# Performance work log

Measured on AMD Instinct MI355X. Metric: run time of the kernel, lower is better.

Reference implementation:

```python
import jax, jax.numpy as jnp
import numpy as np

N = 50000        # nodes
E = 400000       # edges
CHUNK = 100      # per-modality input dim
NCH = 2          # number of chunks (modalities)
OUT = 96         # out_chunks
HID = NCH * OUT  # m_hidden = 192
NCLS = 2         # edge classes
EPS = 1e-5


def layer_norm(x, g, b):
    m = jnp.mean(x, axis=-1, keepdims=True)
    v = jnp.var(x, axis=-1, keepdims=True)
    return (x - m) * jax.lax.rsqrt(v + EPS) * g + b


def setup_inputs() -> dict:
    key = jax.random.key(0)
    ks = jax.random.split(key, 20)
    inp = {}
    inp["h"] = jax.random.normal(ks[0], (N, NCH * CHUNK), dtype=jnp.float32)
    inp["dist"] = jax.random.uniform(ks[1], (E,), dtype=jnp.float32)
    inp["src"] = jax.random.randint(ks[2], (E,), 0, N)
    inp["dst"] = jax.random.randint(ks[3], (E,), 0, N)
    # projector params (equal chunk sizes -> stacked): Linear(100,96)+LayerNorm(96)
    s = 1.0 / np.sqrt(CHUNK)
    inp["proj_W"] = jax.random.uniform(ks[4], (NCH, CHUNK, OUT), minval=-s, maxval=s, dtype=jnp.float32)
    inp["proj_b"] = jax.random.uniform(ks[5], (NCH, OUT), minval=-s, maxval=s, dtype=jnp.float32)
    inp["proj_g"] = jnp.ones((NCH, OUT), jnp.float32)
    inp["proj_beta"] = jnp.zeros((NCH, OUT), jnp.float32)
    # 2 GcnSAGE layers actually run (m_layers-1): Linear(2*192, 192) + LayerNorm(192)
    sg = 1.0 / np.sqrt(2 * HID)
    inp["gcn_W"] = jax.random.uniform(ks[6], (2, 2 * HID, HID), minval=-sg, maxval=sg, dtype=jnp.float32)
    inp["gcn_b"] = jax.random.uniform(ks[7], (2, HID), minval=-sg, maxval=sg, dtype=jnp.float32)
    inp["gcn_g"] = jnp.ones((2, HID), jnp.float32)
    inp["gcn_beta"] = jnp.zeros((2, HID), jnp.float32)
    # edge MLP predictor: 192 -> 96 -> 2
    s1 = 1.0 / np.sqrt(HID)
    s2 = 1.0 / np.sqrt(HID // 2)
    inp["ep_W1"] = jax.random.uniform(ks[8], (HID, HID // 2), minval=-s1, maxval=s1, dtype=jnp.float32)
    inp["ep_b1"] = jax.random.uniform(ks[9], (HID // 2,), minval=-s1, maxval=s1, dtype=jnp.float32)
    inp["ep_W2"] = jax.random.uniform(ks[10], (HID // 2, NCLS), minval=-s2, maxval=s2, dtype=jnp.float32)
    inp["ep_b2"] = jax.random.uniform(ks[11], (NCLS,), minval=-s2, maxval=s2, dtype=jnp.float32)
    return inp


def reference(h, dist, proj_W, proj_b, proj_g, proj_beta,
              gcn_W, gcn_b, gcn_g, gcn_beta,
              ep_W1, ep_b1, ep_W2, ep_b2, src, dst):
    # InputProjector: per-chunk Linear + LayerNorm + LeakyReLU, concat
    x = h.reshape(N, NCH, CHUNK)
    y = jnp.einsum('ncd,cde->nce', x, proj_W) + proj_b
    y = jax.nn.leaky_relu(layer_norm(y, proj_g, proj_beta), negative_slope=0.01)
    hh = y.reshape(N, HID)

    # 1/in_degree norm (inf -> 0)
    deg = jax.ops.segment_sum(jnp.ones((E,), hh.dtype), dst, num_segments=N)
    norm = jnp.where(deg > 0, 1.0 / deg, 0.0)[:, None]

    # m_layers - 1 = 2 GcnSAGE layers: ah = sum_{u->v} h_u * dist_e
    for l in range(2):
        msg = hh[src] * dist[:, None]                       # [E, HID]
        ah = jax.ops.segment_sum(msg, dst, num_segments=N)  # [N, HID]
        hc = jnp.concatenate([hh, ah * norm], axis=1)       # [N, 2*HID]
        hh = hc @ gcn_W[l] + gcn_b[l]
        hh = jax.nn.relu(layer_norm(hh, gcn_g[l], gcn_beta[l]))

    # edge scoring: W2(relu(W1(h_src * h_dst)))
    he = hh[src] * hh[dst]                                   # [E, HID]
    score = jax.nn.relu(he @ ep_W1 + ep_b1) @ ep_W2 + ep_b2  # [E, 2]
    return score
```

## Files before the change

### kernel.cpp

```cpp
#include <hip/hip_runtime.h>
#include <math.h>

#define N_NODES 50000
#define N_EDGES 400000
#define CHUNK   100
#define NCH     2
#define OUTC    96
#define HID     192
#define HID2    384
#define EPS     1e-5f

typedef __bf16 bf16x8 __attribute__((ext_vector_type(8)));
typedef float  f32x4  __attribute__((ext_vector_type(4)));

__device__ inline unsigned short f2bf(float f) {
    unsigned int u = __float_as_uint(f);
    unsigned int r = (u + 0x7FFFu + ((u >> 16) & 1u)) >> 16;
    return (unsigned short)r;
}

#define W1T_SZ (96 * 192)
__global__ void prep_w1t(const float* __restrict__ W1, unsigned short* __restrict__ w1t)
{
    int i = blockIdx.x * 256 + threadIdx.x;
    if (i < W1T_SZ) {
        int j = i / HID, k = i % HID;
        w1t[i] = f2bf(W1[k * OUTC + j]);
    }
}

__global__ __launch_bounds__(192) void proj_kernel(
    const float* __restrict__ h, const float* __restrict__ W,
    const float* __restrict__ b, const float* __restrict__ g,
    const float* __restrict__ beta, float* __restrict__ hh)
{
    __shared__ float xs[16][NCH * CHUNK];
    __shared__ float red[2][16][2][6];
    __shared__ float mv[2][16][2];
    const int tid = threadIdx.x;
    const int nbase = blockIdx.x * 16;

    for (int i = tid; i < 16 * 50; i += 192) {
        int row = i / 50, seg = i % 50;
        int n = nbase + row;
        float4 v = make_float4(0.f, 0.f, 0.f, 0.f);
        if (n < N_NODES) v = *(const float4*)&h[(size_t)n * (NCH * CHUNK) + seg * 4];
        *(float4*)&xs[row][seg * 4] = v;
    }
    __syncthreads();

    const int c = tid / OUTC, j = tid % OUTC;
    const float* wc = &W[c * CHUNK * OUTC];

    float acc[16];
    float bb = b[c * OUTC + j];
    #pragma unroll
    for (int i = 0; i < 16; ++i) acc[i] = bb;

    for (int d = 0; d < CHUNK; d += 4) {
        float w0 = wc[(d + 0) * OUTC + j];
        float w1 = wc[(d + 1) * OUTC + j];
        float w2 = wc[(d + 2) * OUTC + j];
        float w3 = wc[(d + 3) * OUTC + j];
        #pragma unroll
        for (int i = 0; i < 16; ++i) {
            float4 hv = *(const float4*)&xs[i][c * CHUNK + d];
            acc[i] += hv.x * w0 + hv.y * w1 + hv.z * w2 + hv.w * w3;
        }
    }
    __syncthreads();
    float* ys = &xs[0][0];
    #pragma unroll
    for (int i = 0; i < 16; ++i) ys[i * HID + c * OUTC + j] = acc[i];
    __syncthreads();
    {
        int grp = tid / 6, q = tid % 6;
        int gi = grp >> 1, gc = grp & 1;
        float s = 0.f, s2 = 0.f;
        #pragma unroll
        for (int t = 0; t < 16; ++t) {
            float v = ys[gi * HID + gc * OUTC + q + 6 * t];
            s += v; s2 += v * v;
        }
        red[0][gi][gc][q] = s; red[1][gi][gc][q] = s2;
    }
    __syncthreads();
    if (tid < 32) {
        int gi = tid >> 1, gc = tid & 1;
        float s = 0.f, s2 = 0.f;
        #pragma unroll
        for (int q = 0; q < 6; ++q) { s += red[0][gi][gc][q]; s2 += red[1][gi][gc][q]; }
        float mean = s * (1.f / 96.f);
        float var  = s2 * (1.f / 96.f) - mean * mean;
        mv[0][gi][gc] = mean;
        mv[1][gi][gc] = rsqrtf(var + EPS);
    }
    __syncthreads();
    float gg = g[c * OUTC + j], be = beta[c * OUTC + j];
    #pragma unroll
    for (int i = 0; i < 16; ++i) {
        int n = nbase + i;
        if (n < N_NODES) {
            float y = (acc[i] - mv[0][i][c]) * mv[1][i][c] * gg + be;
            y = (y < 0.f) ? 0.01f * y : y;
            hh[(size_t)n * HID + c * OUTC + j] = y;
        }
    }
}

__global__ void zero_deg_kernel(int* __restrict__ deg)
{
    int i = blockIdx.x * blockDim.x + threadIdx.x;
    if (i < N_NODES) deg[i] = 0;
}

__global__ void count_kernel(const int* __restrict__ dst, int* __restrict__ deg)
{
    int e = blockIdx.x * blockDim.x + threadIdx.x;
    if (e < N_EDGES) atomicAdd(&deg[dst[e]], 1);
}

__global__ __launch_bounds__(1024) void scan_kernel(
    const int* __restrict__ deg, int* __restrict__ rowstart,
    int* __restrict__ cursor, float* __restrict__ norm)
{
    __shared__ int sums[1024];
    const int t = threadIdx.x;
    const int L = (N_NODES + 1023) / 1024;
    int lo = t * L, hi = min(lo + L, N_NODES);
    int s = 0;
    for (int i = lo; i < hi; ++i) s += deg[i];
    sums[t] = s;
    __syncthreads();
    if (t == 0) {
        int run = 0;
        for (int i = 0; i < 1024; ++i) { int v = sums[i]; sums[i] = run; run += v; }
        rowstart[N_NODES] = run;
    }
    __syncthreads();
    int off = sums[t];
    for (int i = lo; i < hi; ++i) {
        int d = deg[i];
        rowstart[i] = off;
        cursor[i]   = off;
        norm[i]     = (d > 0) ? 1.f / (float)d : 0.f;
        off += d;
    }
}

__global__ void fill_kernel(const int* __restrict__ src, const int* __restrict__ dst,
                            const float* __restrict__ dist, int* __restrict__ cursor,
                            int* __restrict__ eidx, int* __restrict__ csr_src,
                            float* __restrict__ csr_dist)
{
    int e = blockIdx.x * blockDim.x + threadIdx.x;
    if (e < N_EDGES) {
        int pos = atomicAdd(&cursor[dst[e]], 1);
        eidx[pos]     = e;
        csr_src[pos]  = src[e];
        csr_dist[pos] = dist[e];
    }
}

__global__ __launch_bounds__(256) void aggregate_kernel(
    const float* __restrict__ hh, const int* __restrict__ csr_src,
    const float* __restrict__ csr_dist, const int* __restrict__ rowstart,
    const float* __restrict__ norm, float* __restrict__ ahn)
{
    const int wave = threadIdx.x >> 6;
    const int lane = threadIdx.x & 63;
    const int v = blockIdx.x * 4 + wave;
    if (v >= N_NODES) return;
    const int r0 = rowstart[v], r1 = rowstart[v + 1];
    const bool act = (lane < 48);
    const int g4 = (act ? lane : 0) * 4;

    f32x4 a = (f32x4){0.f, 0.f, 0.f, 0.f};
    int k = r0;
    for (; k + 1 < r1; k += 2) {
        int   s0 = csr_src[k],   s1 = csr_src[k + 1];
        float d0 = csr_dist[k],  d1 = csr_dist[k + 1];
        f32x4 h0 = *(const f32x4*)&hh[(size_t)s0 * HID + g4];
        f32x4 h1 = *(const f32x4*)&hh[(size_t)s1 * HID + g4];
        a += h0 * d0;
        a += h1 * d1;
    }
    if (k < r1) {
        int s0 = csr_src[k];
        float d0 = csr_dist[k];
        f32x4 h0 = *(const f32x4*)&hh[(size_t)s0 * HID + g4];
        a += h0 * d0;
    }
    if (act) {
        float nm = norm[v];
        a *= nm;
        *(f32x4*)&ahn[(size_t)v * HID + g4] = a;
    }
}

__global__ __launch_bounds__(256, 1) void update_kernel(
    float* __restrict__ hh, const float* __restrict__ ahn,
    const float* __restrict__ W, const float* __restrict__ b,
    const float* __restrict__ g, const float* __restrict__ beta)
{
    __shared__ float red[64][4][2];
    const int tid  = threadIdx.x;
    const int lane = tid & 63;
    const int wv   = tid >> 6;
    const int j0   = __builtin_amdgcn_readfirstlane(wv * 48);
    const int node = blockIdx.x * 64 + lane;
    const bool valid = (node < N_NODES);
    const int nclamp = valid ? node : (N_NODES - 1);

    const float* __restrict__ xrow = &hh[(size_t)nclamp * HID];
    const float* __restrict__ arow = &ahn[(size_t)nclamp * HID];

    f32x4 a0, a1, a2, a3, a4, a5, a6, a7, a8, a9, a10, a11;
    {
        const f32x4* bj = (const f32x4*)&b[j0];
        a0 = bj[0]; a1 = bj[1]; a2 = bj[2];  a3 = bj[3];  a4 = bj[4];   a5 = bj[5];
        a6 = bj[6]; a7 = bj[7]; a8 = bj[8];  a9 = bj[9];  a10 = bj[10]; a11 = bj[11];
    }

#define UPD_STEP(xs, krow)                                                   \
    {                                                                        \
        const f32x4* __restrict__ wr = (const f32x4*)&W[(size_t)(krow) * HID + j0]; \
        a0  += (xs) * wr[0];  a1  += (xs) * wr[1];  a2  += (xs) * wr[2];     \
        a3  += (xs) * wr[3];  a4  += (xs) * wr[4];  a5  += (xs) * wr[5];     \
        a6  += (xs) * wr[6];  a7  += (xs) * wr[7];  a8  += (xs) * wr[8];     \
        a9  += (xs) * wr[9];  a10 += (xs) * wr[10]; a11 += (xs) * wr[11];    \
    }

    for (int k = 0; k < HID; k += 4) {
        float4 xv = *(const float4*)&xrow[k];
        UPD_STEP(xv.x, k + 0)
        UPD_STEP(xv.y, k + 1)
        UPD_STEP(xv.z, k + 2)
        UPD_STEP(xv.w, k + 3)
    }
    for (int k = 0; k < HID; k += 4) {
        float4 xv = *(const float4*)&arow[k];
        UPD_STEP(xv.x, HID + k + 0)
        UPD_STEP(xv.y, HID + k + 1)
        UPD_STEP(xv.z, HID + k + 2)
        UPD_STEP(xv.w, HID + k + 3)
    }
#undef UPD_STEP

    float s = 0.f, s2 = 0.f;
#define UPD_SUM(av) { s += av[0] + av[1] + av[2] + av[3];                          \
                      s2 += av[0]*av[0] + av[1]*av[1] + av[2]*av[2] + av[3]*av[3]; }
    UPD_SUM(a0) UPD_SUM(a1) UPD_SUM(a2) UPD_SUM(a3) UPD_SUM(a4) UPD_SUM(a5)
    UPD_SUM(a6) UPD_SUM(a7) UPD_SUM(a8) UPD_SUM(a9) UPD_SUM(a10) UPD_SUM(a11)
#undef UPD_SUM
    red[lane][wv][0] = s;
    red[lane][wv][1] = s2;
    __syncthreads();
    float st = 0.f, s2t = 0.f;
    #pragma unroll
    for (int w2 = 0; w2 < 4; ++w2) { st += red[lane][w2][0]; s2t += red[lane][w2][1]; }
    float mean = st * (1.f / HID);
    float var  = s2t * (1.f / HID) - mean * mean;
    float rstd = rsqrtf(var + EPS);

    if (valid) {
        float* __restrict__ orow = &hh[(size_t)node * HID + j0];
        const f32x4* __restrict__ gj = (const f32x4*)&g[j0];
        const f32x4* __restrict__ ej = (const f32x4*)&beta[j0];
#define UPD_OUT(av, jv)                                                      \
    {                                                                        \
        f32x4 gv = gj[jv], bv = ej[jv], o;                                   \
        o[0] = fmaxf((av[0] - mean) * rstd * gv[0] + bv[0], 0.f);            \
        o[1] = fmaxf((av[1] - mean) * rstd * gv[1] + bv[1], 0.f);            \
        o[2] = fmaxf((av[2] - mean) * rstd * gv[2] + bv[2], 0.f);            \
        o[3] = fmaxf((av[3] - mean) * rstd * gv[3] + bv[3], 0.f);            \
        *(f32x4*)&orow[(jv) * 4] = o;                                        \
    }
        UPD_OUT(a0, 0)  UPD_OUT(a1, 1)  UPD_OUT(a2, 2)  UPD_OUT(a3, 3)
        UPD_OUT(a4, 4)  UPD_OUT(a5, 5)  UPD_OUT(a6, 6)  UPD_OUT(a7, 7)
        UPD_OUT(a8, 8)  UPD_OUT(a9, 9)  UPD_OUT(a10, 10) UPD_OUT(a11, 11)
#undef UPD_OUT
    }
}

__global__ __launch_bounds__(256) void edge_mfma_kernel(
    const float* __restrict__ hh, const int* __restrict__ src, const int* __restrict__ dst,
    const int* __restrict__ eidx,
    const unsigned short* __restrict__ w1t, const float* __restrict__ b1,
    const float* __restrict__ W2, const float* __restrict__ b2,
    float* __restrict__ out)
{
    __shared__ unsigned short he[64][200];
    __shared__ int sidx[64], didx[64], eor[64];
    const int tid = threadIdx.x;
    const int ebase = blockIdx.x * 64;

    if (tid < 64) {
        int e = eidx[ebase + tid];
        eor[tid] = e;
        sidx[tid] = src[e];
        didx[tid] = dst[e];
    }
    __syncthreads();

    for (int idx = tid; idx < 64 * 48; idx += 256) {
        int slot = idx / 48, q = idx % 48;
        f32x4 sv = *(const f32x4*)&hh[(size_t)sidx[slot] * HID + q * 4];
        f32x4 dv = *(const f32x4*)&hh[(size_t)didx[slot] * HID + q * 4];
        f32x4 pv = sv * dv;
        ushort4 o;
        o.x = f2bf(pv[0]); o.y = f2bf(pv[1]); o.z = f2bf(pv[2]); o.w = f2bf(pv[3]);
        *(ushort4*)&he[slot][q * 4] = o;
    }
    __syncthreads();

    const int w    = tid >> 6;
    const int lane = tid & 63;
    const int lo   = lane & 15;
    const int hi   = lane >> 4;

    f32x4 acc[6];
    #pragma unroll
    for (int nt = 0; nt < 6; ++nt) acc[nt] = (f32x4){0.f, 0.f, 0.f, 0.f};

    #pragma unroll
    for (int kt = 0; kt < 6; ++kt) {
        const int k0 = kt * 32 + hi * 8;
        bf16x8 af = *(const bf16x8*)&he[w * 16 + lo][k0];
        #pragma unroll
        for (int nt = 0; nt < 6; ++nt) {
            bf16x8 bfr = *(const bf16x8*)&w1t[(size_t)(nt * 16 + lo) * HID + k0];
            acc[nt] = __builtin_amdgcn_mfma_f32_16x16x32_bf16(af, bfr, acc[nt], 0, 0, 0);
        }
    }

    float b1c[6], w20[6], w21[6];
    #pragma unroll
    for (int nt = 0; nt < 6; ++nt) {
        int col = nt * 16 + lo;
        b1c[nt] = b1[col];
        w20[nt] = W2[col * 2 + 0];
        w21[nt] = W2[col * 2 + 1];
    }
    float bb0 = b2[0], bb1 = b2[1];
    #pragma unroll
    for (int reg = 0; reg < 4; ++reg) {
        float p0 = 0.f, p1 = 0.f;
        #pragma unroll
        for (int nt = 0; nt < 6; ++nt) {
            float hv = fmaxf(acc[nt][reg] + b1c[nt], 0.f);
            p0 += hv * w20[nt];
            p1 += hv * w21[nt];
        }
        #pragma unroll
        for (int off = 1; off < 16; off <<= 1) {
            p0 += __shfl_xor(p0, off, 64);
            p1 += __shfl_xor(p1, off, 64);
        }
        if (lo == 0) {
            int row = hi * 4 + reg;
            int e = eor[w * 16 + row];
            out[(size_t)e * 2 + 0] = p0 + bb0;
            out[(size_t)e * 2 + 1] = p1 + bb1;
        }
    }
}

extern "C" void kernel_launch(void* const* d_in, const int* in_sizes, int n_in,
                              void* d_out, int out_size, void* d_ws, size_t ws_size,
                              hipStream_t stream)
{
    const float* h         = (const float*)d_in[0];
    const float* dist      = (const float*)d_in[1];
    const int*   src       = (const int*)  d_in[2];
    const int*   dst       = (const int*)  d_in[3];
    const float* proj_W    = (const float*)d_in[4];
    const float* proj_b    = (const float*)d_in[5];
    const float* proj_g    = (const float*)d_in[6];
    const float* proj_beta = (const float*)d_in[7];
    const float* gcn_W     = (const float*)d_in[8];
    const float* gcn_b     = (const float*)d_in[9];
    const float* gcn_g     = (const float*)d_in[10];
    const float* gcn_beta  = (const float*)d_in[11];
    const float* ep_W1     = (const float*)d_in[12];
    const float* ep_b1     = (const float*)d_in[13];
    const float* ep_W2     = (const float*)d_in[14];
    const float* ep_b2     = (const float*)d_in[15];
    float* out = (float*)d_out;

    char* p = (char*)d_ws;
    float* hh  = (float*)p;  p += (size_t)N_NODES * HID * sizeof(float);
    float* ahn = (float*)p;  p += (size_t)N_NODES * HID * sizeof(float);
    float* nrm = (float*)p;  p += (size_t)N_NODES * sizeof(float);
    int* deg      = (int*)p; p += (size_t)N_NODES * sizeof(int);
    int* rowstart = (int*)p; p += (size_t)(N_NODES + 1) * sizeof(int);
    int* cursor   = (int*)p; p += (size_t)N_NODES * sizeof(int);
    int* eidx     = (int*)p; p += (size_t)N_EDGES * sizeof(int);
    int* csr_src  = (int*)p; p += (size_t)N_EDGES * sizeof(int);
    float* csr_dist = (float*)p; p += (size_t)N_EDGES * sizeof(float);
    p = (char*)(((uintptr_t)p + 255) & ~(uintptr_t)255);
    unsigned short* w1t = (unsigned short*)p; p += (size_t)W1T_SZ * sizeof(unsigned short);

    prep_w1t<<<(W1T_SZ + 255) / 256, 256, 0, stream>>>(ep_W1, w1t);
    proj_kernel<<<(N_NODES + 15) / 16, 192, 0, stream>>>(
        h, proj_W, proj_b, proj_g, proj_beta, hh);
    zero_deg_kernel<<<(N_NODES + 255) / 256, 256, 0, stream>>>(deg);
    count_kernel<<<(N_EDGES + 255) / 256, 256, 0, stream>>>(dst, deg);
    scan_kernel<<<1, 1024, 0, stream>>>(deg, rowstart, cursor, nrm);
    fill_kernel<<<(N_EDGES + 255) / 256, 256, 0, stream>>>(
        src, dst, dist, cursor, eidx, csr_src, csr_dist);
    for (int l = 0; l < 2; ++l) {
        aggregate_kernel<<<(N_NODES + 3) / 4, 256, 0, stream>>>(
            hh, csr_src, csr_dist, rowstart, nrm, ahn);
        update_kernel<<<(N_NODES + 63) / 64, 256, 0, stream>>>(
            hh, ahn, gcn_W + (size_t)l * HID2 * HID, gcn_b + l * HID,
            gcn_g + l * HID, gcn_beta + l * HID);
    }
    edge_mfma_kernel<<<N_EDGES / 64, 256, 0, stream>>>(
        hh, src, dst, eidx, w1t, ep_b1, ep_W2, ep_b2, out);
}
```

Measured before the change: 750.3 us.

## Split update GEMM K-dimension across two wave groups and unroll aggregation by four

```diff
diff --git a/kernel.cpp b/kernel.cpp
--- a/kernel.cpp
+++ b/kernel.cpp
@@ -177,15 +177,19 @@
 
     f32x4 a = (f32x4){0.f, 0.f, 0.f, 0.f};
     int k = r0;
-    for (; k + 1 < r1; k += 2) {
-        int   s0 = csr_src[k],   s1 = csr_src[k + 1];
-        float d0 = csr_dist[k],  d1 = csr_dist[k + 1];
+    for (; k + 3 < r1; k += 4) {
+        int   s0 = csr_src[k],   s1 = csr_src[k+1],  s2 = csr_src[k+2],  s3 = csr_src[k+3];
+        float d0 = csr_dist[k],  d1 = csr_dist[k+1], d2 = csr_dist[k+2], d3 = csr_dist[k+3];
         f32x4 h0 = *(const f32x4*)&hh[(size_t)s0 * HID + g4];
         f32x4 h1 = *(const f32x4*)&hh[(size_t)s1 * HID + g4];
+        f32x4 h2 = *(const f32x4*)&hh[(size_t)s2 * HID + g4];
+        f32x4 h3 = *(const f32x4*)&hh[(size_t)s3 * HID + g4];
         a += h0 * d0;
         a += h1 * d1;
-    }
-    if (k < r1) {
+        a += h2 * d2;
+        a += h3 * d3;
+    }
+    for (; k < r1; ++k) {
         int s0 = csr_src[k];
         float d0 = csr_dist[k];
         f32x4 h0 = *(const f32x4*)&hh[(size_t)s0 * HID + g4];
@@ -198,28 +202,34 @@
     }
 }
 
-__global__ __launch_bounds__(256, 1) void update_kernel(
+__global__ __launch_bounds__(512) void update_kernel(
     float* __restrict__ hh, const float* __restrict__ ahn,
     const float* __restrict__ W, const float* __restrict__ b,
     const float* __restrict__ g, const float* __restrict__ beta)
 {
+    __shared__ float mrg[4][48][64];
     __shared__ float red[64][4][2];
     const int tid  = threadIdx.x;
     const int lane = tid & 63;
     const int wv   = tid >> 6;
-    const int j0   = __builtin_amdgcn_readfirstlane(wv * 48);
+    const int wb   = wv & 3;
+    const int half = wv >> 2;
+    const int j0   = __builtin_amdgcn_readfirstlane(wb * 48);
     const int node = blockIdx.x * 64 + lane;
     const bool valid = (node < N_NODES);
     const int nclamp = valid ? node : (N_NODES - 1);
 
-    const float* __restrict__ xrow = &hh[(size_t)nclamp * HID];
-    const float* __restrict__ arow = &ahn[(size_t)nclamp * HID];
+    const float* __restrict__ xrow = half ? &ahn[(size_t)nclamp * HID]
+                                          : &hh[(size_t)nclamp * HID];
+    const int kbase = half * HID;
 
     f32x4 a0, a1, a2, a3, a4, a5, a6, a7, a8, a9, a10, a11;
-    {
+    if (half == 0) {
         const f32x4* bj = (const f32x4*)&b[j0];
         a0 = bj[0]; a1 = bj[1]; a2 = bj[2];  a3 = bj[3];  a4 = bj[4];   a5 = bj[5];
         a6 = bj[6]; a7 = bj[7]; a8 = bj[8];  a9 = bj[9];  a10 = bj[10]; a11 = bj[11];
+    } else {
+        a0=a1=a2=a3=a4=a5=a6=a7=a8=a9=a10=a11 = (f32x4){0.f,0.f,0.f,0.f};
     }
 
 #define UPD_STEP(xs, krow)                                                   \
@@ -230,43 +240,57 @@
         a6  += (xs) * wr[6];  a7  += (xs) * wr[7];  a8  += (xs) * wr[8];     \
         a9  += (xs) * wr[9];  a10 += (xs) * wr[10]; a11 += (xs) * wr[11];    \
     }
-
     for (int k = 0; k < HID; k += 4) {
         float4 xv = *(const float4*)&xrow[k];
-        UPD_STEP(xv.x, k + 0)
-        UPD_STEP(xv.y, k + 1)
-        UPD_STEP(xv.z, k + 2)
-        UPD_STEP(xv.w, k + 3)
-    }
-    for (int k = 0; k < HID; k += 4) {
-        float4 xv = *(const float4*)&arow[k];
-        UPD_STEP(xv.x, HID + k + 0)
-        UPD_STEP(xv.y, HID + k + 1)
-        UPD_STEP(xv.z, HID + k + 2)
-        UPD_STEP(xv.w, HID + k + 3)
+        UPD_STEP(xv.x, kbase + k + 0)
+        UPD_STEP(xv.y, kbase + k + 1)
+        UPD_STEP(xv.z, kbase + k + 2)
+        UPD_STEP(xv.w, kbase + k + 3)
     }
 #undef UPD_STEP
 
-    float s = 0.f, s2 = 0.f;
+    if (half == 1) {
+#define UPD_DUMP(av, jv)                                                     \
+        mrg[wb][(jv)*4+0][lane] = av[0]; mrg[wb][(jv)*4+1][lane] = av[1];    \
+        mrg[wb][(jv)*4+2][lane] = av[2]; mrg[wb][(jv)*4+3][lane] = av[3];
+        UPD_DUMP(a0, 0)  UPD_DUMP(a1, 1)  UPD_DUMP(a2, 2)  UPD_DUMP(a3, 3)
+        UPD_DUMP(a4, 4)  UPD_DUMP(a5, 5)  UPD_DUMP(a6, 6)  UPD_DUMP(a7, 7)
+        UPD_DUMP(a8, 8)  UPD_DUMP(a9, 9)  UPD_DUMP(a10, 10) UPD_DUMP(a11, 11)
+#undef UPD_DUMP
+    }
+    __syncthreads();
+
+    if (half == 0) {
+#define UPD_MERGE(av, jv)                                                    \
+        av[0] += mrg[wb][(jv)*4+0][lane]; av[1] += mrg[wb][(jv)*4+1][lane];  \
+        av[2] += mrg[wb][(jv)*4+2][lane]; av[3] += mrg[wb][(jv)*4+3][lane];
+        UPD_MERGE(a0, 0)  UPD_MERGE(a1, 1)  UPD_MERGE(a2, 2)  UPD_MERGE(a3, 3)
+        UPD_MERGE(a4, 4)  UPD_MERGE(a5, 5)  UPD_MERGE(a6, 6)  UPD_MERGE(a7, 7)
+        UPD_MERGE(a8, 8)  UPD_MERGE(a9, 9)  UPD_MERGE(a10, 10) UPD_MERGE(a11, 11)
+#undef UPD_MERGE
+        float s = 0.f, s2 = 0.f;
 #define UPD_SUM(av) { s += av[0] + av[1] + av[2] + av[3];                          \
                       s2 += av[0]*av[0] + av[1]*av[1] + av[2]*av[2] + av[3]*av[3]; }
-    UPD_SUM(a0) UPD_SUM(a1) UPD_SUM(a2) UPD_SUM(a3) UPD_SUM(a4) UPD_SUM(a5)
-    UPD_SUM(a6) UPD_SUM(a7) UPD_SUM(a8) UPD_SUM(a9) UPD_SUM(a10) UPD_SUM(a11)
+        UPD_SUM(a0) UPD_SUM(a1) UPD_SUM(a2) UPD_SUM(a3) UPD_SUM(a4) UPD_SUM(a5)
+        UPD_SUM(a6) UPD_SUM(a7) UPD_SUM(a8) UPD_SUM(a9) UPD_SUM(a10) UPD_SUM(a11)
 #undef UPD_SUM
-    red[lane][wv][0] = s;
-    red[lane][wv][1] = s2;
-    __syncthreads();
-    float st = 0.f, s2t = 0.f;
-    #pragma unroll
-    for (int w2 = 0; w2 < 4; ++w2) { st += red[lane][w2][0]; s2t += red[lane][w2][1]; }
-    float mean = st * (1.f / HID);
-    float var  = s2t * (1.f / HID) - mean * mean;
-    float rstd = rsqrtf(var + EPS);
-
-    if (valid) {
-        float* __restrict__ orow = &hh[(size_t)node * HID + j0];
-        const f32x4* __restrict__ gj = (const f32x4*)&g[j0];
-        const f32x4* __restrict__ ej = (const f32x4*)&beta[j0];
+        red[lane][wb][0] = s;
+        red[lane][wb][1] = s2;
+    }
+    __syncthreads();
+
+    if (half == 0) {
+        float st = 0.f, s2t = 0.f;
+        #pragma unroll
+        for (int w2 = 0; w2 < 4; ++w2) { st += red[lane][w2][0]; s2t += red[lane][w2][1]; }
+        float mean = st * (1.f / HID);
+        float var  = s2t * (1.f / HID) - mean * mean;
+        float rstd = rsqrtf(var + EPS);
+
+        if (valid) {
+            float* __restrict__ orow = &hh[(size_t)node * HID + j0];
+            const f32x4* __restrict__ gj = (const f32x4*)&g[j0];
+            const f32x4* __restrict__ ej = (const f32x4*)&beta[j0];
 #define UPD_OUT(av, jv)                                                      \
     {                                                                        \
         f32x4 gv = gj[jv], bv = ej[jv], o;                                   \
@@ -276,10 +300,11 @@
         o[3] = fmaxf((av[3] - mean) * rstd * gv[3] + bv[3], 0.f);            \
         *(f32x4*)&orow[(jv) * 4] = o;                                        \
     }
-        UPD_OUT(a0, 0)  UPD_OUT(a1, 1)  UPD_OUT(a2, 2)  UPD_OUT(a3, 3)
-        UPD_OUT(a4, 4)  UPD_OUT(a5, 5)  UPD_OUT(a6, 6)  UPD_OUT(a7, 7)
-        UPD_OUT(a8, 8)  UPD_OUT(a9, 9)  UPD_OUT(a10, 10) UPD_OUT(a11, 11)
+            UPD_OUT(a0, 0)  UPD_OUT(a1, 1)  UPD_OUT(a2, 2)  UPD_OUT(a3, 3)
+            UPD_OUT(a4, 4)  UPD_OUT(a5, 5)  UPD_OUT(a6, 6)  UPD_OUT(a7, 7)
+            UPD_OUT(a8, 8)  UPD_OUT(a9, 9)  UPD_OUT(a10, 10) UPD_OUT(a11, 11)
 #undef UPD_OUT
+        }
     }
 }
 
@@ -412,7 +437,7 @@
     for (int l = 0; l < 2; ++l) {
         aggregate_kernel<<<(N_NODES + 3) / 4, 256, 0, stream>>>(
             hh, csr_src, csr_dist, rowstart, nrm, ahn);
-        update_kernel<<<(N_NODES + 63) / 64, 256, 0, stream>>>(
+        update_kernel<<<(N_NODES + 63) / 64, 512, 0, stream>>>(
             hh, ahn, gcn_W + (size_t)l * HID2 * HID, gcn_b + l * HID,
             gcn_g + l * HID, gcn_beta + l * HID);
     }
```

After: 1.594 ms. 112% more time.
